# Kernel tuning notes

Hardware: AMD Instinct MI355X
Metric: run time of the kernel (lower is better)

Reference implementation:

```python
import jax, jax.numpy as jnp
import numpy as np

# Config constants from the W-Net paper (Config() in the original repo)
RADIUS = 5.0
SIGMA_X = 4.0
SIGMA_I = 10.0
PAD = 5  # window offsets dm, dn in [-5, 4] (torch.arange exclusive upper bound)

# Precompute the static list of active window offsets.
# Original: if dist < radius -> w = 0; else w = (dist^2 / -sigma_x) * (||dx|| / -sigma_i)
# (the two negatives cancel, so w = dist^2/sigma_x * ||dx||/sigma_i).
_OFFSETS = []
for dm in range(-5, 5):
    for dn in range(-5, 5):
        d2 = dm * dm + dn * dn
        if np.sqrt(d2) >= RADIUS:  # NOTE: faithful to the (inverted-looking) source condition
            _OFFSETS.append((dm, dn, d2 / SIGMA_X))


def setup_inputs() -> dict:
    key = jax.random.key(0)
    k1, k2 = jax.random.split(key)
    N, K, X, Y, C = 8, 20, 224, 224, 3
    seg = jax.random.uniform(k1, (N, K, X, Y), dtype=jnp.float32)
    x = jax.random.uniform(k2, (N, C, X, Y), dtype=jnp.float32)
    return {"seg": seg, "x": x}


def reference(seg, x):
    N, K, X, Y = seg.shape
    Kconst = jnp.float32(K)
    xi = jnp.transpose(x, (0, 2, 3, 1))  # [N, X, Y, C], matches x[idx].transpose(0,2).transpose(0,1)

    # Zero padding: out-of-window pixels get seg=0, killing their contribution,
    # which exactly reproduces the max(0,.)/min(X,.) loop bounds.
    xp = jnp.pad(xi, ((0, 0), (PAD, PAD), (PAD, PAD), (0, 0)))
    sp = jnp.pad(seg, ((0, 0), (0, 0), (PAD, PAD), (PAD, PAD)))

    # assocA[n,k,i,j] = seg[n,k,i,j] * sum_{dm,dn} w(i,j,i+dm,j+dn) * seg[n,k,i+dm,j+dn]
    accA = jnp.zeros((N, K), dtype=seg.dtype)
    for dm, dn, sw in _OFFSETS:  # static, ~31 offsets
        xs = jax.lax.dynamic_slice(xp, (0, PAD + dm, PAD + dn, 0), (N, X, Y, xi.shape[-1]))
        ss = jax.lax.dynamic_slice(sp, (0, 0, PAD + dm, PAD + dn), (N, K, X, Y))
        diffn = jnp.linalg.norm(xi - xs, axis=-1)  # [N, X, Y], ||xi[i,j]-xi[m,n]||_2
        w = (jnp.float32(sw)) * (diffn / jnp.float32(SIGMA_I))  # [N, X, Y]
        accA = accA + jnp.sum(seg * (w[:, None] * ss), axis=(2, 3))
    assocA_sum = accA  # [N, K]

    # assocV[n,k,i,j] = seg[n,k,i,j] * sum_{m,n'} ||xi[i,j] - xi[m,n']||^2
    # expand: XY*||xi[i,j]||^2 - 2 xi[i,j].S + sum ||xi||^2
    sq = jnp.sum(xi * xi, axis=-1)               # [N, X, Y]
    s2 = jnp.sum(sq, axis=(1, 2))                # [N]
    S = jnp.sum(xi, axis=(1, 2))                 # [N, C]
    npix = jnp.float32(X * Y)
    temp = npix * sq - 2.0 * jnp.einsum('nxyc,nc->nxy', xi, S) + s2[:, None, None]
    assocV_sum = jnp.einsum('nkxy,nxy->nk', seg, temp)  # [N, K]

    Nassoc = assocA_sum / assocV_sum             # [N, K]
    loss = jnp.sum(Kconst - jnp.sum(Nassoc, axis=1))  # sum over batch
    return loss.reshape(1)
```

## Files before the change

### kernel.cpp

```cpp
#include <hip/hip_runtime.h>

#define NB 8
#define KK 20
#define XD 224
#define YD 224
#define NPIX (XD*YD)
#define TILE 16
#define NT 14
#define TW 26
#define NOFF 31
#define NKTOT (NB*KK)
#define NTILES (NT*NT)
#define NPH 3
#define KPH 7
#define SB 32

namespace {
constexpr int DM[NOFF] = {
  -5,-5,-5,-5,-5,-5,-5,-5,-5,-5,
  -4,-4,-4,-4,-4,
  -3,-3,-3,
  -2,-1, 0, 1, 2,
   3, 3, 3,
   4, 4, 4, 4, 4};
constexpr int DN[NOFF] = {
  -5,-4,-3,-2,-1, 0, 1, 2, 3, 4,
  -5,-4,-3, 3, 4,
  -5,-4, 4,
  -5,-5,-5,-5,-5,
  -5,-4, 4,
  -5,-4,-3, 3, 4};

constexpr int ROFXI[NOFF] = {
  (DM[0]+5)*TW+(DN[0]+5),  (DM[1]+5)*TW+(DN[1]+5),  (DM[2]+5)*TW+(DN[2]+5),
  (DM[3]+5)*TW+(DN[3]+5),  (DM[4]+5)*TW+(DN[4]+5),  (DM[5]+5)*TW+(DN[5]+5),
  (DM[6]+5)*TW+(DN[6]+5),  (DM[7]+5)*TW+(DN[7]+5),  (DM[8]+5)*TW+(DN[8]+5),
  (DM[9]+5)*TW+(DN[9]+5),  (DM[10]+5)*TW+(DN[10]+5),(DM[11]+5)*TW+(DN[11]+5),
  (DM[12]+5)*TW+(DN[12]+5),(DM[13]+5)*TW+(DN[13]+5),(DM[14]+5)*TW+(DN[14]+5),
  (DM[15]+5)*TW+(DN[15]+5),(DM[16]+5)*TW+(DN[16]+5),(DM[17]+5)*TW+(DN[17]+5),
  (DM[18]+5)*TW+(DN[18]+5),(DM[19]+5)*TW+(DN[19]+5),(DM[20]+5)*TW+(DN[20]+5),
  (DM[21]+5)*TW+(DN[21]+5),(DM[22]+5)*TW+(DN[22]+5),(DM[23]+5)*TW+(DN[23]+5),
  (DM[24]+5)*TW+(DN[24]+5),(DM[25]+5)*TW+(DN[25]+5),(DM[26]+5)*TW+(DN[26]+5),
  (DM[27]+5)*TW+(DN[27]+5),(DM[28]+5)*TW+(DN[28]+5),(DM[29]+5)*TW+(DN[29]+5),
  (DM[30]+5)*TW+(DN[30]+5)};
constexpr float COSC[NOFF] = {
  (DM[0]*DM[0]+DN[0]*DN[0])/40.0f,   (DM[1]*DM[1]+DN[1]*DN[1])/40.0f,
  (DM[2]*DM[2]+DN[2]*DN[2])/40.0f,   (DM[3]*DM[3]+DN[3]*DN[3])/40.0f,
  (DM[4]*DM[4]+DN[4]*DN[4])/40.0f,   (DM[5]*DM[5]+DN[5]*DN[5])/40.0f,
  (DM[6]*DM[6]+DN[6]*DN[6])/40.0f,   (DM[7]*DM[7]+DN[7]*DN[7])/40.0f,
  (DM[8]*DM[8]+DN[8]*DN[8])/40.0f,   (DM[9]*DM[9]+DN[9]*DN[9])/40.0f,
  (DM[10]*DM[10]+DN[10]*DN[10])/40.0f,(DM[11]*DM[11]+DN[11]*DN[11])/40.0f,
  (DM[12]*DM[12]+DN[12]*DN[12])/40.0f,(DM[13]*DM[13]+DN[13]*DN[13])/40.0f,
  (DM[14]*DM[14]+DN[14]*DN[14])/40.0f,(DM[15]*DM[15]+DN[15]*DN[15])/40.0f,
  (DM[16]*DM[16]+DN[16]*DN[16])/40.0f,(DM[17]*DM[17]+DN[17]*DN[17])/40.0f,
  (DM[18]*DM[18]+DN[18]*DN[18])/40.0f,(DM[19]*DM[19]+DN[19]*DN[19])/40.0f,
  (DM[20]*DM[20]+DN[20]*DN[20])/40.0f,(DM[21]*DM[21]+DN[21]*DN[21])/40.0f,
  (DM[22]*DM[22]+DN[22]*DN[22])/40.0f,(DM[23]*DM[23]+DN[23]*DN[23])/40.0f,
  (DM[24]*DM[24]+DN[24]*DN[24])/40.0f,(DM[25]*DM[25]+DN[25]*DN[25])/40.0f,
  (DM[26]*DM[26]+DN[26]*DN[26])/40.0f,(DM[27]*DM[27]+DN[27]*DN[27])/40.0f,
  (DM[28]*DM[28]+DN[28]*DN[28])/40.0f,(DM[29]*DM[29]+DN[29]*DN[29])/40.0f,
  (DM[30]*DM[30]+DN[30]*DN[30])/40.0f};
}

__global__ void ncuts_stats1(const float* __restrict__ x, float* __restrict__ part) {
  __shared__ float red[4][4];
  const int b = blockIdx.x;
  const int n = b >> 5, s = b & 31;
  const int t = threadIdx.x;
  const int lane = t & 63, wv = t >> 6;
  const float* xb = x + n * 3 * NPIX;
  const int base = s * (NPIX / SB);
  float a0 = 0.f, a1 = 0.f, a2 = 0.f, aq = 0.f;
  for (int i = t; i < NPIX / SB; i += 256) {
    const int p = base + i;
    float v0 = xb[p], v1 = xb[NPIX + p], v2 = xb[2 * NPIX + p];
    a0 += v0; a1 += v1; a2 += v2;
    aq = fmaf(v0, v0, fmaf(v1, v1, fmaf(v2, v2, aq)));
  }
  #pragma unroll
  for (int m = 1; m < 64; m <<= 1) {
    a0 += __shfl_xor(a0, m, 64); a1 += __shfl_xor(a1, m, 64);
    a2 += __shfl_xor(a2, m, 64); aq += __shfl_xor(aq, m, 64);
  }
  if (lane == 0) { red[wv][0] = a0; red[wv][1] = a1; red[wv][2] = a2; red[wv][3] = aq; }
  __syncthreads();
  if (t < 4) part[b * 4 + t] = red[0][t] + red[1][t] + red[2][t] + red[3][t];
}

__global__ void ncuts_stats2(const float* __restrict__ part,
                             float* __restrict__ Sv, float* __restrict__ s2v) {
  const int t = threadIdx.x;
  if (t < NB * 4) {
    const int n = t >> 2, val = t & 3;
    float s = 0.f;
    #pragma unroll 4
    for (int i = 0; i < SB; ++i) s += part[(n * SB + i) * 4 + val];
    if (val < 3) Sv[n * 3 + val] = s; else s2v[n] = s;
  }
}

__global__ __launch_bounds__(256, 4)
void ncuts_main(const float* __restrict__ seg, const float* __restrict__ x,
                const float* __restrict__ Sv, const float* __restrict__ s2v,
                float* __restrict__ pA, float* __restrict__ pV) {
  __shared__ __align__(16) float sSegA[TW*TW*4];
  __shared__ __align__(16) float sSegB[TW*TW*4];
  __shared__ __align__(16) float sXi[TW*TW*4];
  __shared__ float sRed[4][48];

  const int t = threadIdx.x;
  const int lane = t & 63, wv = t >> 6;
  const int tx = t & 15, ty = t >> 4;
  const int tcx = blockIdx.x, tcy = blockIdx.y, n = blockIdx.z;
  const int r0 = tcy * TILE - 5, c0 = tcx * TILE - 5;

  const float* xb = x + n * 3 * NPIX;
  for (int e = t; e < TW * TW; e += 256) {
    const int rr = e / TW, cc = e - rr * TW;
    const int gr = r0 + rr, gc = c0 + cc;
    float v0 = 0.f, v1 = 0.f, v2 = 0.f;
    if ((unsigned)gr < XD && (unsigned)gc < YD) {
      const int g = gr * YD + gc;
      v0 = xb[g]; v1 = xb[NPIX + g]; v2 = xb[2 * NPIX + g];
    }
    *reinterpret_cast<float4*>(&sXi[e * 4]) = make_float4(v0, v1, v2, 0.f);
  }

  const float* sb = seg + n * KK * NPIX;
  const float* psb[3]; bool pok[3];
  #pragma unroll
  for (int s = 0; s < 3; ++s) {
    const int p = t + s * 256;
    const int rr = p / TW, cc = p - rr * TW;
    const int gr = r0 + rr, gc = c0 + cc;
    pok[s] = (p < TW * TW) && ((unsigned)gr < XD) && ((unsigned)gc < YD);
    psb[s] = sb + (gr * YD + gc);
  }

  const int xib = ty * TW + tx;
  const int cen = xib + (5 * TW + 5);

  const float S0 = Sv[n*3+0], S1 = Sv[n*3+1], S2 = Sv[n*3+2], s2n = s2v[n];

  float xc0, xc1, xc2, temp;
  bool haveCenter = false;

  #pragma unroll 1
  for (int p = 0; p < NPH; ++p) {
    const int kbase = p * KPH;
    const int kcnt  = (p == NPH - 1) ? (KK - 2 * KPH) : KPH;

    __syncthreads();

    #pragma unroll
    for (int s = 0; s < 3; ++s) {
      const int pix = t + s * 256;
      if (pix < TW * TW) {
        float v[8];
        #pragma unroll
        for (int ks = 0; ks < 8; ++ks) v[ks] = 0.f;
        if (pok[s]) {
          #pragma unroll
          for (int ks = 0; ks < KPH; ++ks)
            if (ks < kcnt) v[ks] = psb[s][(kbase + ks) * NPIX];
        }
        *reinterpret_cast<float4*>(&sSegA[pix * 4]) = make_float4(v[0], v[1], v[2], v[3]);
        *reinterpret_cast<float4*>(&sSegB[pix * 4]) = make_float4(v[4], v[5], v[6], v[7]);
      }
    }
    __syncthreads();

    if (!haveCenter) {
      const float4 xc = *reinterpret_cast<const float4*>(&sXi[cen * 4]);
      xc0 = xc.x; xc1 = xc.y; xc2 = xc.z;
      const float sqc = xc0*xc0 + xc1*xc1 + xc2*xc2;
      temp = 50176.f * sqc - 2.f * (xc0*S0 + xc1*S1 + xc2*S2) + s2n;
      haveCenter = true;
    }

    float acc[8];
    #pragma unroll
    for (int k = 0; k < 8; ++k) acc[k] = 0.f;

    #pragma unroll 2
    for (int o = 0; o < NOFF; ++o) {
      const int rof = ROFXI[o];
      const float4 xs = *reinterpret_cast<const float4*>(&sXi[(xib + rof) * 4]);
      const float d0 = xc0 - xs.x, d1 = xc1 - xs.y, d2 = xc2 - xs.z;
      const float w = COSC[o] * sqrtf(fmaf(d0, d0, fmaf(d1, d1, d2 * d2)));
      const float4 q0 = *reinterpret_cast<const float4*>(&sSegA[(xib + rof) * 4]);
      const float4 q1 = *reinterpret_cast<const float4*>(&sSegB[(xib + rof) * 4]);
      acc[0] = fmaf(w, q0.x, acc[0]); acc[1] = fmaf(w, q0.y, acc[1]);
      acc[2] = fmaf(w, q0.z, acc[2]); acc[3] = fmaf(w, q0.w, acc[3]);
      acc[4] = fmaf(w, q1.x, acc[4]); acc[5] = fmaf(w, q1.y, acc[5]);
      acc[6] = fmaf(w, q1.z, acc[6]); acc[7] = fmaf(w, q1.w, acc[7]);
    }

    const float4 c0v = *reinterpret_cast<const float4*>(&sSegA[cen * 4]);
    const float4 c1v = *reinterpret_cast<const float4*>(&sSegB[cen * 4]);
    const float segc[8] = {c0v.x, c0v.y, c0v.z, c0v.w, c1v.x, c1v.y, c1v.z, c1v.w};

    #pragma unroll
    for (int pp = 0; pp < 4; ++pp) {
      const int s0i = 2 * pp, s1i = 2 * pp + 1;
      float pa0 = segc[s0i] * acc[s0i], pv0 = segc[s0i] * temp;
      float pa1 = segc[s1i] * acc[s1i], pv1 = segc[s1i] * temp;
      float s0 = (lane & 1) ? pv0 : pa0;
      float g0 = (lane & 1) ? pa0 : pv0;
      s0 += __shfl_xor(g0, 1, 64);
      float s1 = (lane & 1) ? pv1 : pa1;
      float g1 = (lane & 1) ? pa1 : pv1;
      s1 += __shfl_xor(g1, 1, 64);
      float cv = (lane & 2) ? s1 : s0;
      float gv = (lane & 2) ? s0 : s1;
      cv += __shfl_xor(gv, 2, 64);
      cv += __shfl_xor(cv, 4, 64);
      cv += __shfl_xor(cv, 8, 64);
      cv += __shfl_xor(cv, 16, 64);
      cv += __shfl_xor(cv, 32, 64);
      const int k0g = kbase + 2 * pp;
      if (lane < 4) sRed[wv][2 * k0g + lane] = cv;
    }
  }

  __syncthreads();
  if (t < 2 * KK) {
    const float s = sRed[0][t] + sRed[1][t] + sRed[2][t] + sRed[3][t];
    const int tile = tcy * NT + tcx;
    const int k = t >> 1;
    float* dst = (t & 1) ? pV : pA;
    dst[tile * NKTOT + n * KK + k] = s;
  }
}

__global__ void ncuts_final(const float* __restrict__ pA, const float* __restrict__ pV,
                            float* __restrict__ out) {
  __shared__ float rA[4][NKTOT];
  __shared__ float rV[4][NKTOT];
  __shared__ float red[256];
  const int t = threadIdx.x;
  const int grp = t >> 8, i = t & 255;
  if (i < NKTOT) {
    float a = 0.f, v = 0.f;
    #pragma unroll 7
    for (int j = 0; j < NTILES / 4; ++j) {
      const int tile = grp * (NTILES / 4) + j;
      a += pA[tile * NKTOT + i];
      v += pV[tile * NKTOT + i];
    }
    rA[grp][i] = a; rV[grp][i] = v;
  }
  __syncthreads();
  if (t < 256) {
    float r = 0.f;
    if (t < NKTOT) {
      const float a = rA[0][t] + rA[1][t] + rA[2][t] + rA[3][t];
      const float v = rV[0][t] + rV[1][t] + rV[2][t] + rV[3][t];
      r = a / v;
    }
    red[t] = r;
  }
  __syncthreads();
  for (int s = 128; s > 0; s >>= 1) {
    if (t < s) red[t] += red[t + s];
    __syncthreads();
  }
  if (t == 0) out[0] = (float)NKTOT - red[0];
}

extern "C" void kernel_launch(void* const* d_in, const int* in_sizes, int n_in,
                              void* d_out, int out_size, void* d_ws, size_t ws_size,
                              hipStream_t stream) {
  const float* seg = (const float*)d_in[0];
  const float* x   = (const float*)d_in[1];
  float* ws   = (float*)d_ws;
  float* pA   = ws;
  float* pV   = ws + NTILES * NKTOT;
  float* Sv   = ws + 2 * NTILES * NKTOT;
  float* s2v  = Sv + 24;
  float* part = s2v + 8;

  ncuts_stats1<<<NB * SB, 256, 0, stream>>>(x, part);
  ncuts_stats2<<<1, 64, 0, stream>>>(part, Sv, s2v);
  dim3 grid(NT, NT, NB);
  ncuts_main<<<grid, 256, 0, stream>>>(seg, x, Sv, s2v, pA, pV);
  ncuts_final<<<1, 1024, 0, stream>>>(pA, pV, (float*)d_out);
}
```

Baseline: 148.4 us.

## Process segments in two phases of ten and split final reduction across blocks

The main kernel now processes the 20 segment channels in two phases of 10 instead of three phases of 7. This cuts the number of sync/reload passes and the number of redundant loads of the window offsets, at the cost of more registers and an extra shared buffer. The sqrt in the weight is replaced by dd*rsqrt(max(dd,eps)), and the center pixel is computed once up front. The final reduction is split into a 160-block per-(n,k) kernel over a transposed partial layout, followed by a small final kernel, replacing the single 1024-thread block.

```diff
diff --git a/kernel.cpp b/kernel.cpp
--- a/kernel.cpp
+++ b/kernel.cpp
@@ -11,8 +11,8 @@
 #define NOFF 31
 #define NKTOT (NB*KK)
 #define NTILES (NT*NT)
-#define NPH 3
-#define KPH 7
+#define NPH 2
+#define KPH 10
 #define SB 32
 
 namespace {
@@ -105,8 +105,9 @@
                 float* __restrict__ pA, float* __restrict__ pV) {
   __shared__ __align__(16) float sSegA[TW*TW*4];
   __shared__ __align__(16) float sSegB[TW*TW*4];
+  __shared__ __align__(16) float sSegC[TW*TW*2];
   __shared__ __align__(16) float sXi[TW*TW*4];
-  __shared__ float sRed[4][48];
+  __shared__ float sRed[4][2*KK];
 
   const int t = threadIdx.x;
   const int lane = t & 63, wv = t >> 6;
@@ -142,13 +143,15 @@
 
   const float S0 = Sv[n*3+0], S1 = Sv[n*3+1], S2 = Sv[n*3+2], s2n = s2v[n];
 
-  float xc0, xc1, xc2, temp;
-  bool haveCenter = false;
+  __syncthreads();
+  const float4 xc = *reinterpret_cast<const float4*>(&sXi[cen * 4]);
+  const float xc0 = xc.x, xc1 = xc.y, xc2 = xc.z;
+  const float sqc = xc0*xc0 + xc1*xc1 + xc2*xc2;
+  const float temp = 50176.f * sqc - 2.f * (xc0*S0 + xc1*S1 + xc2*S2) + s2n;
 
   #pragma unroll 1
   for (int p = 0; p < NPH; ++p) {
     const int kbase = p * KPH;
-    const int kcnt  = (p == NPH - 1) ? (KK - 2 * KPH) : KPH;
 
     __syncthreads();
 
@@ -156,52 +159,49 @@
     for (int s = 0; s < 3; ++s) {
       const int pix = t + s * 256;
       if (pix < TW * TW) {
-        float v[8];
+        float v[KPH];
         #pragma unroll
-        for (int ks = 0; ks < 8; ++ks) v[ks] = 0.f;
+        for (int ks = 0; ks < KPH; ++ks) v[ks] = 0.f;
         if (pok[s]) {
           #pragma unroll
-          for (int ks = 0; ks < KPH; ++ks)
-            if (ks < kcnt) v[ks] = psb[s][(kbase + ks) * NPIX];
+          for (int ks = 0; ks < KPH; ++ks) v[ks] = psb[s][(kbase + ks) * NPIX];
         }
         *reinterpret_cast<float4*>(&sSegA[pix * 4]) = make_float4(v[0], v[1], v[2], v[3]);
         *reinterpret_cast<float4*>(&sSegB[pix * 4]) = make_float4(v[4], v[5], v[6], v[7]);
+        *reinterpret_cast<float2*>(&sSegC[pix * 2]) = make_float2(v[8], v[9]);
       }
     }
     __syncthreads();
 
-    if (!haveCenter) {
-      const float4 xc = *reinterpret_cast<const float4*>(&sXi[cen * 4]);
-      xc0 = xc.x; xc1 = xc.y; xc2 = xc.z;
-      const float sqc = xc0*xc0 + xc1*xc1 + xc2*xc2;
-      temp = 50176.f * sqc - 2.f * (xc0*S0 + xc1*S1 + xc2*S2) + s2n;
-      haveCenter = true;
-    }
-
-    float acc[8];
+    float acc[KPH];
     #pragma unroll
-    for (int k = 0; k < 8; ++k) acc[k] = 0.f;
+    for (int k = 0; k < KPH; ++k) acc[k] = 0.f;
 
     #pragma unroll 2
     for (int o = 0; o < NOFF; ++o) {
       const int rof = ROFXI[o];
       const float4 xs = *reinterpret_cast<const float4*>(&sXi[(xib + rof) * 4]);
       const float d0 = xc0 - xs.x, d1 = xc1 - xs.y, d2 = xc2 - xs.z;
-      const float w = COSC[o] * sqrtf(fmaf(d0, d0, fmaf(d1, d1, d2 * d2)));
+      const float dd = fmaf(d0, d0, fmaf(d1, d1, d2 * d2));
+      const float w = COSC[o] * dd * __frsqrt_rn(fmaxf(dd, 1e-30f));
       const float4 q0 = *reinterpret_cast<const float4*>(&sSegA[(xib + rof) * 4]);
       const float4 q1 = *reinterpret_cast<const float4*>(&sSegB[(xib + rof) * 4]);
+      const float2 q2 = *reinterpret_cast<const float2*>(&sSegC[(xib + rof) * 2]);
       acc[0] = fmaf(w, q0.x, acc[0]); acc[1] = fmaf(w, q0.y, acc[1]);
       acc[2] = fmaf(w, q0.z, acc[2]); acc[3] = fmaf(w, q0.w, acc[3]);
       acc[4] = fmaf(w, q1.x, acc[4]); acc[5] = fmaf(w, q1.y, acc[5]);
       acc[6] = fmaf(w, q1.z, acc[6]); acc[7] = fmaf(w, q1.w, acc[7]);
+      acc[8] = fmaf(w, q2.x, acc[8]); acc[9] = fmaf(w, q2.y, acc[9]);
     }
 
     const float4 c0v = *reinterpret_cast<const float4*>(&sSegA[cen * 4]);
     const float4 c1v = *reinterpret_cast<const float4*>(&sSegB[cen * 4]);
-    const float segc[8] = {c0v.x, c0v.y, c0v.z, c0v.w, c1v.x, c1v.y, c1v.z, c1v.w};
+    const float2 c2v = *reinterpret_cast<const float2*>(&sSegC[cen * 2]);
+    const float segc[KPH] = {c0v.x, c0v.y, c0v.z, c0v.w,
+                             c1v.x, c1v.y, c1v.z, c1v.w, c2v.x, c2v.y};
 
     #pragma unroll
-    for (int pp = 0; pp < 4; ++pp) {
+    for (int pp = 0; pp < KPH / 2; ++pp) {
       const int s0i = 2 * pp, s1i = 2 * pp + 1;
       float pa0 = segc[s0i] * acc[s0i], pv0 = segc[s0i] * temp;
       float pa1 = segc[s1i] * acc[s1i], pv1 = segc[s1i] * temp;
@@ -229,37 +229,33 @@
     const int tile = tcy * NT + tcx;
     const int k = t >> 1;
     float* dst = (t & 1) ? pV : pA;
-    dst[tile * NKTOT + n * KK + k] = s;
-  }
-}
-
-__global__ void ncuts_final(const float* __restrict__ pA, const float* __restrict__ pV,
-                            float* __restrict__ out) {
-  __shared__ float rA[4][NKTOT];
-  __shared__ float rV[4][NKTOT];
+    dst[(n * KK + k) * NTILES + tile] = s;
+  }
+}
+
+__global__ void ncuts_final1(const float* __restrict__ pA, const float* __restrict__ pV,
+                             float* __restrict__ rA, float* __restrict__ rV) {
+  const int nk = blockIdx.x, t = threadIdx.x;
+  float a = 0.f, v = 0.f;
+  for (int j = t; j < NTILES; j += 64) {
+    a += pA[nk * NTILES + j];
+    v += pV[nk * NTILES + j];
+  }
+  #pragma unroll
+  for (int m = 1; m < 64; m <<= 1) {
+    a += __shfl_xor(a, m, 64);
+    v += __shfl_xor(v, m, 64);
+  }
+  if (t == 0) { rA[nk] = a; rV[nk] = v; }
+}
+
+__global__ void ncuts_final2(const float* __restrict__ rA, const float* __restrict__ rV,
+                             float* __restrict__ out) {
   __shared__ float red[256];
   const int t = threadIdx.x;
-  const int grp = t >> 8, i = t & 255;
-  if (i < NKTOT) {
-    float a = 0.f, v = 0.f;
-    #pragma unroll 7
-    for (int j = 0; j < NTILES / 4; ++j) {
-      const int tile = grp * (NTILES / 4) + j;
-      a += pA[tile * NKTOT + i];
-      v += pV[tile * NKTOT + i];
-    }
-    rA[grp][i] = a; rV[grp][i] = v;
-  }
-  __syncthreads();
-  if (t < 256) {
-    float r = 0.f;
-    if (t < NKTOT) {
-      const float a = rA[0][t] + rA[1][t] + rA[2][t] + rA[3][t];
-      const float v = rV[0][t] + rV[1][t] + rV[2][t] + rV[3][t];
-      r = a / v;
-    }
-    red[t] = r;
-  }
+  float r = 0.f;
+  if (t < NKTOT) r = rA[t] / rV[t];
+  red[t] = r;
   __syncthreads();
   for (int s = 128; s > 0; s >>= 1) {
     if (t < s) red[t] += red[t + s];
@@ -275,14 +271,17 @@
   const float* x   = (const float*)d_in[1];
   float* ws   = (float*)d_ws;
   float* pA   = ws;
-  float* pV   = ws + NTILES * NKTOT;
-  float* Sv   = ws + 2 * NTILES * NKTOT;
+  float* pV   = ws + NKTOT * NTILES;
+  float* Sv   = ws + 2 * NKTOT * NTILES;
   float* s2v  = Sv + 24;
   float* part = s2v + 8;
+  float* rA   = part + 1024;
+  float* rV   = rA + NKTOT;
 
   ncuts_stats1<<<NB * SB, 256, 0, stream>>>(x, part);
   ncuts_stats2<<<1, 64, 0, stream>>>(part, Sv, s2v);
   dim3 grid(NT, NT, NB);
   ncuts_main<<<grid, 256, 0, stream>>>(seg, x, Sv, s2v, pA, pV);
-  ncuts_final<<<1, 1024, 0, stream>>>(pA, pV, (float*)d_out);
-}
+  ncuts_final1<<<NKTOT, 64, 0, stream>>>(pA, pV, rA, rV);
+  ncuts_final2<<<1, 256, 0, stream>>>(rA, rV, (float*)d_out);
+}
```

New measurement: 131.8 us. 11.2% less time.
